# Kernel tuning notes

Measured on AMD Instinct MI355X. Metric: run time of the kernel, lower is better.

## Reference

```python
import jax, jax.numpy as jnp
import numpy as np

L, E, H, S, V, F = 8, 1024, 16, 2048, 32000, 4096
NEG = -1e9  # mask value used by the original (triu * -1e9)


def setup_inputs() -> dict:
    key = jax.random.key(0)
    ks = jax.random.split(key, 10)
    s = 0.02  # init scale to keep activations stable without residuals/LN
    return {
        "inpt": jax.random.randint(ks[0], (S,), 0, V, dtype=jnp.int32),
        "num_heads": H,
        "emb_table": jax.random.normal(ks[1], (V, E), dtype=jnp.float32) * s,
        "Wq": jax.random.normal(ks[2], (L, E, E), dtype=jnp.float32) * s,
        "bq": jnp.zeros((L, E), dtype=jnp.float32),
        "Wk": jax.random.normal(ks[3], (L, E, E), dtype=jnp.float32) * s,
        "bk": jnp.zeros((L, E), dtype=jnp.float32),
        "Wv": jax.random.normal(ks[4], (L, E, E), dtype=jnp.float32) * s,
        "bv": jnp.zeros((L, E), dtype=jnp.float32),
        "W1": jax.random.normal(ks[5], (L, E, F), dtype=jnp.float32) * s,
        "b1": jnp.zeros((L, F), dtype=jnp.float32),
        "W2": jax.random.normal(ks[6], (L, F, E), dtype=jnp.float32) * s,
        "b2": jnp.zeros((L, E), dtype=jnp.float32),
        "Wout": jax.random.normal(ks[7], (E, V), dtype=jnp.float32) * s,
    }


def reference(inpt, num_heads, emb_table, Wq, bq, Wk, bk, Wv, bv, W1, b1, W2, b2, Wout):
    x = emb_table[inpt]                      # [S, E] embedding lookup
    seq_len, emb_dim = x.shape
    head_dim = emb_dim // num_heads
    scale = head_dim ** 0.5
    n_layers = Wq.shape[0]
    # additive causal mask, exactly as torch.triu(ones)*-1e9
    mask = jnp.triu(jnp.full((seq_len, seq_len), NEG, dtype=x.dtype), k=1)

    for l in range(n_layers):  # fixed small layer count
        q = (x @ Wq[l] + bq[l]).reshape(seq_len, num_heads, head_dim).transpose(1, 0, 2)
        k = (x @ Wk[l] + bk[l]).reshape(seq_len, num_heads, head_dim).transpose(1, 0, 2)
        v = (x @ Wv[l] + bv[l]).reshape(seq_len, num_heads, head_dim).transpose(1, 0, 2)
        scores = jnp.einsum('hqd,hkd->hqk', q, k) / scale + mask  # [H, S, S]
        probs = jax.nn.softmax(scores, axis=-1)
        attn = jnp.einsum('hqk,hkd->hqd', probs, v)               # [H, S, D]
        attn = attn.transpose(1, 0, 2).reshape(seq_len, emb_dim)  # [S, E]
        # NOTE: original has no residual connection; x is replaced by FFN(attn)
        x = jax.nn.relu(attn @ W1[l] + b1[l]) @ W2[l] + b2[l]

    return x @ Wout  # [S, V] logits (no bias, no softmax in original forward)
```

## Files before the change

kernel.cpp:

```cpp
#include <hip/hip_runtime.h>
#include <hip/hip_fp16.h>


#define SS 2048
#define EE 1024
#define NH 16
#define FF 4096
#define NV 32000
#define NL 8

typedef _Float16 f16;
typedef _Float16 f16x8 __attribute__((ext_vector_type(8)));
typedef _Float16 f16x4 __attribute__((ext_vector_type(4)));
typedef float f32x4 __attribute__((ext_vector_type(4)));
typedef float f32x16 __attribute__((ext_vector_type(16)));

#define CS 4096.0f
#define INV_CS 0.000244140625f
#define SCORE_SCALE 7.450580596923828e-09f

__device__ __forceinline__ void gload16(const void* g, void* lds) {
    __builtin_amdgcn_global_load_lds(
        (const __attribute__((address_space(1))) unsigned int*)g,
        (__attribute__((address_space(3))) unsigned int*)lds, 16, 0, 0);
}

#define BAR do { asm volatile("" ::: "memory"); __builtin_amdgcn_s_barrier(); } while (0)

__global__ void k_embed(const int* __restrict__ ids, const float* __restrict__ emb,
                        f16* __restrict__ xh) {
    int s = blockIdx.x;
    int e = threadIdx.x * 4;
    const float4 v = *(const float4*)&emb[(size_t)ids[s] * EE + e];
    f16x4 h;
    h[0] = (f16)(v.x * CS); h[1] = (f16)(v.y * CS);
    h[2] = (f16)(v.z * CS); h[3] = (f16)(v.w * CS);
    *(f16x4*)&xh[(size_t)s * EE + e] = h;
}

__device__ __forceinline__ void tr64(const float* __restrict__ in, f16* __restrict__ out,
                                     int ldi, int ldo, int bx, int by) {
    __shared__ float tl[64][65];
    const int tx = threadIdx.x & 15, ty = threadIdx.x >> 4;
#pragma unroll
    for (int i = 0; i < 4; i++) {
        float4 v = *(const float4*)&in[(size_t)(by + ty * 4 + i) * ldi + bx + tx * 4];
        tl[ty * 4 + i][tx * 4 + 0] = v.x;
        tl[ty * 4 + i][tx * 4 + 1] = v.y;
        tl[ty * 4 + i][tx * 4 + 2] = v.z;
        tl[ty * 4 + i][tx * 4 + 3] = v.w;
    }
    __syncthreads();
#pragma unroll
    for (int i = 0; i < 4; i++) {
        f16x4 h;
#pragma unroll
        for (int j = 0; j < 4; j++) h[j] = (f16)tl[tx * 4 + j][ty * 4 + i];
        *(f16x4*)&out[(size_t)(bx + ty * 4 + i) * ldo + by + tx * 4] = h;
    }
}

__global__ void k_trW(const float* __restrict__ Wq, const float* __restrict__ Wk,
                      const float* __restrict__ Wv, const float* __restrict__ W1,
                      const float* __restrict__ W2,
                      const float* __restrict__ bq, const float* __restrict__ bk,
                      const float* __restrict__ bv,
                      f16* __restrict__ wqkvt, f16* __restrict__ w1t,
                      f16* __restrict__ w2t, float* __restrict__ bqkv) {
    int b = blockIdx.x;
    if (b == 2816) {
        int i = threadIdx.x;
#pragma unroll
        for (int j = 0; j < 12; j++) {
            int idx = j * 256 + i;
            bqkv[idx] = idx < EE ? bq[idx] : (idx < 2 * EE ? bk[idx - EE] : bv[idx - 2 * EE]);
        }
        return;
    }
    if (b < 768) {
        int s = b >> 8, t2 = b & 255;
        tr64(s == 0 ? Wq : (s == 1 ? Wk : Wv), wqkvt + (size_t)s * EE * EE,
             EE, EE, (t2 & 15) * 64, (t2 >> 4) * 64);
    } else if (b < 1792) {
        int t2 = b - 768;
        tr64(W1, w1t, FF, EE, (t2 & 63) * 64, (t2 >> 6) * 64);
    } else {
        int t2 = b - 1792;
        tr64(W2, w2t, EE, FF, (t2 & 15) * 64, (t2 >> 4) * 64);
    }
}

__global__ void k_trOut(const float* __restrict__ in, f16* __restrict__ out) {
    int b = blockIdx.x;
    tr64(in, out, NV, EE, (b % 500) * 64, (b / 500) * 64);
}

__global__ void k_combine4(const float* __restrict__ part, const float* __restrict__ bias,
                           f16* __restrict__ out) {
    const size_t sz = (size_t)SS * EE;
    int i = (blockIdx.x * 256 + threadIdx.x) * 4;
    float4 a = *(const float4*)&part[i];
    float4 b = *(const float4*)&part[i + sz];
    float4 c = *(const float4*)&part[i + 2 * sz];
    float4 d = *(const float4*)&part[i + 3 * sz];
    float4 bb = *(const float4*)&bias[i & (EE - 1)];
    f16x4 h;
    h[0] = (f16)(a.x + b.x + c.x + d.x + bb.x * CS);
    h[1] = (f16)(a.y + b.y + c.y + d.y + bb.y * CS);
    h[2] = (f16)(a.z + b.z + c.z + d.z + bb.z * CS);
    h[3] = (f16)(a.w + b.w + c.w + d.w + bb.w * CS);
    *(f16x4*)&out[i] = h;
}

template<int BM, int BN, int TAG>
__global__ __launch_bounds__((BM == 128) ? 256 : 512, 2) void k_gemm(
    const f16* __restrict__ A, const f16* __restrict__ B,
    const float* __restrict__ bias, f16* __restrict__ Ch, float* __restrict__ Cf,
    f16* __restrict__ VtOut,
    int M, int N, int Kstride, int Ksub, int nm, int nn, int kch,
    float bscale, float oscale, int relu) {
    constexpr int WR = (BM == 256) ? ((BN == 256) ? 2 : 4) : 2;
    constexpr int WC = (BN == 256) ? 4 : 2;
    constexpr int NW = WR * WC;
    constexpr int THREADS = NW * 64;
    constexpr int MR = BM / WR / 16;
    constexpr int RPC = THREADS / 8;
    constexpr int ACALLS = BM / RPC;
    constexpr int BCALLS = BN / RPC;
    constexpr int LPT = ACALLS + BCALLS;

    __shared__ f16 As[2][BM * 64];
    __shared__ f16 Bs[2][BN * 64];

    const int t = threadIdx.x;
    const int l = t & 63, w = t >> 6;
    const int lr = l & 15, lc = l >> 4;

    const int nwg = nm * nn * kch;
    const int q8 = nwg >> 3, r8 = nwg & 7;
    const int xcd = blockIdx.x & 7, lid = blockIdx.x >> 3;
    const int wgid = (xcd < r8 ? xcd * (q8 + 1) : r8 * (q8 + 1) + (xcd - r8) * q8) + lid;
    const int kc = wgid / (nm * nn);
    const int rem = wgid - kc * (nm * nn);
    const int m0 = (rem % nm) * BM, n0 = (rem / nm) * BN;

    const f16* Ab = A + (size_t)kc * Ksub;
    const f16* Bb = B + (size_t)kc * Ksub;
    float* Cfb = Cf ? Cf + (size_t)kc * M * N : nullptr;

    const int wr = w / WC, wc = w % WC;

    f32x4 acc[MR][4] = {};

    const int srow = t >> 3;
    const int scol = 8 * ((t & 7) ^ (srow & 7));
    const int NT = Ksub / 64;

#define STAGE(bb, tt_) { \
    const size_t kof = (size_t)(tt_) * 64 + scol; \
    _Pragma("unroll") \
    for (int c = 0; c < ACALLS; c++) \
        gload16(Ab + (size_t)(m0 + c * RPC + srow) * Kstride + kof, \
                (char*)As[bb] + c * (RPC * 128) + w * 1024); \
    _Pragma("unroll") \
    for (int c = 0; c < BCALLS; c++) \
        gload16(Bb + (size_t)(n0 + c * RPC + srow) * Kstride + kof, \
                (char*)Bs[bb] + c * (RPC * 128) + w * 1024); }

    STAGE(0, 0)
    STAGE(1, 1)
    asm volatile("s_waitcnt vmcnt(%0)" :: "n"(LPT) : "memory");
    BAR;

    int cur = 0;
    for (int tt = 0; tt < NT; ++tt) {
        const f16* pA = As[cur];
        const f16* pB = Bs[cur];
#pragma unroll
        for (int ks = 0; ks < 2; ks++) {
            f16x8 af[MR], bf[4];
#pragma unroll
            for (int m = 0; m < MR; m++) {
                const int row = wr * (MR * 16) + m * 16 + lr;
                af[m] = *(const f16x8*)&pA[row * 64 + 8 * ((ks * 4 + lc) ^ (row & 7))];
            }
#pragma unroll
            for (int n = 0; n < 4; n++) {
                const int row = wc * 64 + n * 16 + lr;
                bf[n] = *(const f16x8*)&pB[row * 64 + 8 * ((ks * 4 + lc) ^ (row & 7))];
            }
            __builtin_amdgcn_s_setprio(1);
#pragma unroll
            for (int m = 0; m < MR; m++)
#pragma unroll
                for (int n = 0; n < 4; n++)
                    acc[m][n] = __builtin_amdgcn_mfma_f32_16x16x32_f16(af[m], bf[n], acc[m][n], 0, 0, 0);
            __builtin_amdgcn_s_setprio(0);
        }
        BAR;
        if (tt + 2 < NT) {
            STAGE(cur, tt + 2)
            asm volatile("s_waitcnt vmcnt(%0)" :: "n"(LPT) : "memory");
        } else if (tt + 1 < NT) {
            asm volatile("s_waitcnt vmcnt(0)" ::: "memory");
        }
        BAR;
        cur ^= 1;
    }
#undef STAGE

#pragma unroll
    for (int m = 0; m < MR; m++)
#pragma unroll
        for (int n = 0; n < 4; n++) {
            const int row0 = m0 + wr * (MR * 16) + m * 16 + lc * 4;
            const int col = n0 + wc * 64 + n * 16 + lr;
            float v[4];
#pragma unroll
            for (int r = 0; r < 4; r++) {
                v[r] = acc[m][n][r];
                if (bias) v[r] += bias[col] * bscale;
                if (relu) v[r] = fmaxf(v[r], 0.0f);
            }
            if (VtOut && col >= 2 * EE) {
                f16x4 h4;
#pragma unroll
                for (int r = 0; r < 4; r++) h4[r] = (f16)v[r];
                *(f16x4*)&VtOut[(size_t)(col - 2 * EE) * SS + row0] = h4;
            } else if (Ch) {
#pragma unroll
                for (int r = 0; r < 4; r++)
                    Ch[(size_t)(row0 + r) * N + col] = (f16)v[r];
            } else {
#pragma unroll
                for (int r = 0; r < 4; r++)
                    Cfb[(size_t)(row0 + r) * N + col] = v[r] * oscale;
            }
        }
}

__global__ __launch_bounds__(512, 2) void k_gemm32(
    const f16* __restrict__ A, const f16* __restrict__ B, float* __restrict__ Cf,
    int N, int Kstride, int nm, int nn, float oscale) {
    __shared__ f16 As[2][256 * 64];
    __shared__ f16 Bs[2][256 * 64];
    const int t = threadIdx.x;
    const int l = t & 63, w = t >> 6;
    const int ln = l & 31, hi = l >> 5;

    const int nwg = nm * nn;
    const int q8 = nwg >> 3, r8 = nwg & 7;
    const int xcd = blockIdx.x & 7, lid = blockIdx.x >> 3;
    const int wgid = (xcd < r8 ? xcd * (q8 + 1) : r8 * (q8 + 1) + (xcd - r8) * q8) + lid;
    const int m0 = (wgid % nm) * 256, n0 = (wgid / nm) * 256;

    const int wr = w >> 2, wc = w & 3;
    f32x16 acc[4][2] = {};

    const int srow = t >> 3;
    const int scol = 8 * ((t & 7) ^ (srow & 7));
    const int NT = Kstride / 64;

#define STAGE32(bb, tt_) { \
    const size_t kof = (size_t)(tt_) * 64 + scol; \
    _Pragma("unroll") \
    for (int c = 0; c < 4; c++) { \
        gload16(A + (size_t)(m0 + c * 64 + srow) * Kstride + kof, \
                (char*)As[bb] + c * 8192 + w * 1024); \
        gload16(B + (size_t)(n0 + c * 64 + srow) * Kstride + kof, \
                (char*)Bs[bb] + c * 8192 + w * 1024); } }

    STAGE32(0, 0)
    STAGE32(1, 1)
    asm volatile("s_waitcnt vmcnt(8)" ::: "memory");
    BAR;

    int cur = 0;
    for (int tt = 0; tt < NT; ++tt) {
        const f16* pA = As[cur];
        const f16* pB = Bs[cur];
#pragma unroll
        for (int ks = 0; ks < 4; ks++) {
            f16x8 af[4], bf[2];
#pragma unroll
            for (int m = 0; m < 4; m++) {
                const int row = wr * 128 + m * 32 + ln;
                af[m] = *(const f16x8*)&pA[row * 64 + 8 * ((ks * 2 + hi) ^ (row & 7))];
            }
#pragma unroll
            for (int n = 0; n < 2; n++) {
                const int row = wc * 64 + n * 32 + ln;
                bf[n] = *(const f16x8*)&pB[row * 64 + 8 * ((ks * 2 + hi) ^ (row & 7))];
            }
            __builtin_amdgcn_s_setprio(1);
#pragma unroll
            for (int m = 0; m < 4; m++)
#pragma unroll
                for (int n = 0; n < 2; n++)
                    acc[m][n] = __builtin_amdgcn_mfma_f32_32x32x16_f16(af[m], bf[n], acc[m][n], 0, 0, 0);
            __builtin_amdgcn_s_setprio(0);
        }
        BAR;
        if (tt + 2 < NT) {
            STAGE32(cur, tt + 2)
            asm volatile("s_waitcnt vmcnt(8)" ::: "memory");
        } else if (tt + 1 < NT) {
            asm volatile("s_waitcnt vmcnt(0)" ::: "memory");
        }
        BAR;
        cur ^= 1;
    }
#undef STAGE32

#pragma unroll
    for (int m = 0; m < 4; m++)
#pragma unroll
        for (int n = 0; n < 2; n++)
#pragma unroll
            for (int r = 0; r < 16; r++) {
                const int row = m0 + wr * 128 + m * 32 + (r & 3) + 8 * (r >> 2) + 4 * hi;
                const int col = n0 + wc * 64 + n * 32 + ln;
                Cf[(size_t)row * N + col] = acc[m][n][r] * oscale;
            }
}

__global__ __launch_bounds__(256) void k_flash(
    const f16* __restrict__ qkv, const f16* __restrict__ vt, f16* __restrict__ attn) {
    __shared__ f16 Ks[2][4096];
    __shared__ f16 Vs[2][4096];
    __shared__ f16 Ps[4096];
    const int h = blockIdx.x;
    const int qb = (SS / 64 - 1) - blockIdx.y;
    const int t = threadIdx.x, l = t & 63, w = t >> 6;
    const int lr = l & 15, lc = l >> 4;
    const int q0 = qb * 64;
    const int qrow = q0 + w * 16 + lr;

    f16x8 qf0 = *(const f16x8*)&qkv[(size_t)qrow * 3072 + h * 64 + lc * 8];
    f16x8 qf1 = *(const f16x8*)&qkv[(size_t)qrow * 3072 + h * 64 + 32 + lc * 8];

    f32x4 o[4] = {};
    float mrun[4], lrun[4];
#pragma unroll
    for (int r = 0; r < 4; r++) { mrun[r] = -__builtin_inff(); lrun[r] = 0.0f; }

    const int krow = t >> 3;
    const int kscol = 8 * ((t & 7) ^ (krow & 7));
    const f16* gK = qkv + EE + h * 64;
    const f16* gV = vt + (size_t)(h * 64) * SS;
    f16* Pw = &Ps[w * 16 * 64];
    const int psw = (lr & 7) << 4;

#define FSTAGE(bb, kt_) { \
    char* dK = (char*)Ks[bb] + w * 1024; \
    char* dV = (char*)Vs[bb] + w * 1024; \
    gload16(gK + (size_t)((kt_) * 64 + krow) * 3072 + kscol, dK); \
    gload16(gK + (size_t)((kt_) * 64 + krow + 32) * 3072 + kscol, dK + 4096); \
    gload16(gV + (size_t)krow * SS + (kt_) * 64 + kscol, dV); \
    gload16(gV + (size_t)(krow + 32) * SS + (kt_) * 64 + kscol, dV + 4096); }

    const int nkt = qb + 1;
    FSTAGE(0, 0)
    FSTAGE(1, 1)
    asm volatile("s_waitcnt vmcnt(4)" ::: "memory");
    __builtin_amdgcn_s_barrier();

    int cur = 0;
    for (int kt = 0; kt < nkt; kt++) {
        f32x4 sc[4];
        __builtin_amdgcn_s_setprio(1);
#pragma unroll
        for (int kj = 0; kj < 4; kj++) {
            const int krw = kj * 16 + lr;
            const int sw = krw & 7;
            f16x8 kb0 = *(const f16x8*)&Ks[cur][krw * 64 + 8 * (lc ^ sw)];
            f16x8 kb1 = *(const f16x8*)&Ks[cur][krw * 64 + 8 * ((lc + 4) ^ sw)];
            f32x4 z = {};
            z = __builtin_amdgcn_mfma_f32_16x16x32_f16(qf0, kb0, z, 0, 0, 0);
            z = __builtin_amdgcn_mfma_f32_16x16x32_f16(qf1, kb1, z, 0, 0, 0);
            sc[kj] = z;
        }
        __builtin_amdgcn_s_setprio(0);

        const bool diag = (kt == qb);
#pragma unroll
        for (int kj = 0; kj < 4; kj++)
#pragma unroll
            for (int r = 0; r < 4; r++) {
                float v = sc[kj][r] * SCORE_SCALE;
                if (diag) {
                    int qq = w * 16 + lc * 4 + r;
                    int kk = kj * 16 + lr;
                    if (kk > qq) v = -__builtin_inff();
                }
                sc[kj][r] = v;
            }

#pragma unroll
        for (int r = 0; r < 4; r++) {
            float mt = fmaxf(fmaxf(sc[0][r], sc[1][r]), fmaxf(sc[2][r], sc[3][r]));
            mt = fmaxf(mt, __shfl_xor(mt, 1));
            mt = fmaxf(mt, __shfl_xor(mt, 2));
            mt = fmaxf(mt, __shfl_xor(mt, 4));
            mt = fmaxf(mt, __shfl_xor(mt, 8));
            float mnew = fmaxf(mrun[r], mt);
            float alpha = __expf(mrun[r] - mnew);
            float psum = 0.0f;
#pragma unroll
            for (int kj = 0; kj < 4; kj++) {
                float p = __expf(sc[kj][r] - mnew);
                sc[kj][r] = p;
                psum += p;
            }
            psum += __shfl_xor(psum, 1);
            psum += __shfl_xor(psum, 2);
            psum += __shfl_xor(psum, 4);
            psum += __shfl_xor(psum, 8);
            lrun[r] = lrun[r] * alpha + psum;
            mrun[r] = mnew;
#pragma unroll
            for (int dj = 0; dj < 4; dj++) o[dj][r] *= alpha;
        }

#pragma unroll
        for (int kj = 0; kj < 4; kj++)
#pragma unroll
            for (int r = 0; r < 4; r++) {
                int prow = lc * 4 + r;
                int pb = prow * 128 + ((kj * 16 + lr) * 2 ^ ((prow & 7) << 4));
                *(f16*)((char*)Pw + pb) = (f16)sc[kj][r];
            }

        __builtin_amdgcn_s_setprio(1);
#pragma unroll
        for (int s2 = 0; s2 < 2; s2++) {
            f16x8 pa = *(const f16x8*)((const char*)Pw + lr * 128 + (((lc + 4 * s2) * 16) ^ psw));
#pragma unroll
            for (int dj = 0; dj < 4; dj++) {
                const int vrow = dj * 16 + lr;
                f16x8 vb = *(const f16x8*)&Vs[cur][vrow * 64 + 8 * ((lc + 4 * s2) ^ (vrow & 7))];
                o[dj] = __builtin_amdgcn_mfma_f32_16x16x32_f16(pa, vb, o[dj], 0, 0, 0);
            }
        }
        __builtin_amdgcn_s_setprio(0);

        asm volatile("" ::: "memory");
        __builtin_amdgcn_s_barrier();
        if (kt + 2 < nkt) {
            FSTAGE(cur, kt + 2)
            asm volatile("s_waitcnt vmcnt(4)" ::: "memory");
        } else if (kt + 1 < nkt) {
            asm volatile("s_waitcnt vmcnt(0)" ::: "memory");
        }
        __builtin_amdgcn_s_barrier();
        cur ^= 1;
    }
#undef FSTAGE

#pragma unroll
    for (int dj = 0; dj < 4; dj++)
#pragma unroll
        for (int r = 0; r < 4; r++) {
            float v = o[dj][r] / lrun[r];
            attn[(size_t)(q0 + w * 16 + lc * 4 + r) * EE + h * 64 + dj * 16 + lr] = (f16)v;
        }
}

extern "C" void kernel_launch(void* const* d_in, const int* in_sizes, int n_in,
                              void* d_out, int out_size, void* d_ws, size_t ws_size,
                              hipStream_t stream) {
    const int*   ids  = (const int*)d_in[0];
    const float* emb  = (const float*)d_in[2];
    const float* Wq   = (const float*)d_in[3];
    const float* bq   = (const float*)d_in[4];
    const float* Wk   = (const float*)d_in[5];
    const float* bk   = (const float*)d_in[6];
    const float* Wv   = (const float*)d_in[7];
    const float* bv   = (const float*)d_in[8];
    const float* W1   = (const float*)d_in[9];
    const float* b1   = (const float*)d_in[10];
    const float* W2   = (const float*)d_in[11];
    const float* b2   = (const float*)d_in[12];
    const float* Wout = (const float*)d_in[13];
    float* out = (float*)d_out;

    char* p = (char*)d_ws;
    f16* xh    = (f16*)p; p += (size_t)SS * EE * 2;
    f16* qkvh  = (f16*)p; p += (size_t)SS * 3 * EE * 2;
    f16* vt    = (f16*)p; p += (size_t)EE * SS * 2;
    f16* attn  = (f16*)p; p += (size_t)SS * EE * 2;
    f16* h1    = (f16*)p; p += (size_t)SS * FF * 2;
    f16* wqkvt = (f16*)p; p += (size_t)3 * EE * EE * 2;
    f16* w1t   = (f16*)p; p += (size_t)FF * EE * 2;
    f16* w2t   = (f16*)p; p += (size_t)EE * FF * 2;
    f16* woutt = (f16*)p; p += (size_t)NV * EE * 2;
    float* part = (float*)p; p += (size_t)4 * SS * EE * 4;
    float* bqkv = (float*)p; p += 3 * EE * 4;

    k_embed<<<SS, 256, 0, stream>>>(ids, emb, xh);

    for (int l = 0; l < NL; l++) {
        k_trW<<<2817, 256, 0, stream>>>(
            Wq + (size_t)l * EE * EE, Wk + (size_t)l * EE * EE, Wv + (size_t)l * EE * EE,
            W1 + (size_t)l * EE * FF, W2 + (size_t)l * FF * EE,
            bq + l * EE, bk + l * EE, bv + l * EE,
            wqkvt, w1t, w2t, bqkv);

        k_gemm<256, 128, 1><<<8 * 24, 512, 0, stream>>>(
            xh, wqkvt, bqkv, qkvh, nullptr, vt, SS, 3 * EE, EE, EE, 8, 24, 1, CS, 1.0f, 0);

        k_flash<<<dim3(NH, SS / 64), 256, 0, stream>>>(qkvh, vt, attn);

        k_gemm<256, 128, 2><<<8 * 32, 512, 0, stream>>>(
            attn, w1t, b1 + (size_t)l * FF, h1, nullptr, nullptr, SS, FF, EE, EE, 8, 32, 1, CS, 1.0f, 1);

        k_gemm<256, 128, 3><<<8 * 8 * 4, 512, 0, stream>>>(
            h1, w2t, nullptr, nullptr, part, nullptr, SS, EE, FF, FF / 4, 8, 8, 4, 0.0f, 1.0f, 0);
        k_combine4<<<SS * EE / 1024, 256, 0, stream>>>(part, b2 + (size_t)l * EE, xh);
    }

    k_trOut<<<8000, 256, 0, stream>>>(Wout, woutt);
    k_gemm32<<<8 * 125, 512, 0, stream>>>(xh, woutt, out, NV, EE, 8, 125, INV_CS);
}
```

Baseline: 1.540 ms.

## Rewrite output GEMM as four-phase pipelined 16x16 MFMA kernel

The final vocabulary-projection GEMM switches from 32x32x16 MFMAs to 16x16x32 MFMAs. The per-tile loop is split into four barrier-separated phases that interleave LDS fragment loads, pieces of the next tile's global-to-LDS staging, and MFMA blocks. The aim is to overlap memory traffic with matrix math and reduce stalls in this large GEMM. The cost is more barriers per K-tile and a different accumulator layout, which may raise register pressure.

```diff
diff --git a/kernel.cpp b/kernel.cpp
--- a/kernel.cpp
+++ b/kernel.cpp
@@ -13,7 +13,6 @@
 typedef _Float16 f16x8 __attribute__((ext_vector_type(8)));
 typedef _Float16 f16x4 __attribute__((ext_vector_type(4)));
 typedef float f32x4 __attribute__((ext_vector_type(4)));
-typedef float f32x16 __attribute__((ext_vector_type(16)));
 
 #define CS 4096.0f
 #define INV_CS 0.000244140625f
@@ -239,14 +238,14 @@
         }
 }
 
-__global__ __launch_bounds__(512, 2) void k_gemm32(
+__global__ __launch_bounds__(512, 2) void k_gemm4p(
     const f16* __restrict__ A, const f16* __restrict__ B, float* __restrict__ Cf,
-    int N, int Kstride, int nm, int nn, float oscale) {
+    int N, int K, int nm, int nn, float oscale) {
     __shared__ f16 As[2][256 * 64];
     __shared__ f16 Bs[2][256 * 64];
     const int t = threadIdx.x;
     const int l = t & 63, w = t >> 6;
-    const int ln = l & 31, hi = l >> 5;
+    const int lr = l & 15, lc = l >> 4;
 
     const int nwg = nm * nn;
     const int q8 = nwg >> 3, r8 = nwg & 7;
@@ -255,23 +254,45 @@
     const int m0 = (wgid % nm) * 256, n0 = (wgid / nm) * 256;
 
     const int wr = w >> 2, wc = w & 3;
-    f32x16 acc[4][2] = {};
+
+    f32x4 acc[8][4] = {};
+    f16x8 aF[2][4], bF[2][4];
 
     const int srow = t >> 3;
     const int scol = 8 * ((t & 7) ^ (srow & 7));
-    const int NT = Kstride / 64;
-
-#define STAGE32(bb, tt_) { \
-    const size_t kof = (size_t)(tt_) * 64 + scol; \
-    _Pragma("unroll") \
-    for (int c = 0; c < 4; c++) { \
-        gload16(A + (size_t)(m0 + c * 64 + srow) * Kstride + kof, \
-                (char*)As[bb] + c * 8192 + w * 1024); \
-        gload16(B + (size_t)(n0 + c * 64 + srow) * Kstride + kof, \
-                (char*)Bs[bb] + c * 8192 + w * 1024); } }
-
-    STAGE32(0, 0)
-    STAGE32(1, 1)
+    const int NT = K / 64;
+
+#define SG_A(bb, tt_, c) \
+    gload16(A + (size_t)(m0 + (c) * 64 + srow) * K + (size_t)(tt_) * 64 + scol, \
+            (char*)As[bb] + (c) * 8192 + w * 1024);
+#define SG_B(bb, tt_, c) \
+    gload16(B + (size_t)(n0 + (c) * 64 + srow) * K + (size_t)(tt_) * 64 + scol, \
+            (char*)Bs[bb] + (c) * 8192 + w * 1024);
+
+#define LDA_HALF(pA_, mh) { _Pragma("unroll") \
+    for (int ks = 0; ks < 2; ks++) _Pragma("unroll") \
+    for (int m = 0; m < 4; m++) { \
+        const int row = wr * 128 + ((mh) * 4 + m) * 16 + lr; \
+        aF[ks][m] = *(const f16x8*)&pA_[row * 64 + 8 * ((ks * 4 + lc) ^ (row & 7))]; } }
+
+#define LDB_PAIR(pB_, nb) { _Pragma("unroll") \
+    for (int ks = 0; ks < 2; ks++) _Pragma("unroll") \
+    for (int j = 0; j < 2; j++) { \
+        const int row = wc * 64 + ((nb) + j) * 16 + lr; \
+        bF[ks][(nb) + j] = *(const f16x8*)&pB_[row * 64 + 8 * ((ks * 4 + lc) ^ (row & 7))]; } }
+
+#define PH_MMA(mb, nb) { __builtin_amdgcn_s_setprio(1); \
+    _Pragma("unroll") for (int ks = 0; ks < 2; ks++) \
+    _Pragma("unroll") for (int m = 0; m < 4; m++) \
+    _Pragma("unroll") for (int j = 0; j < 2; j++) \
+        acc[(mb) + m][(nb) + j] = __builtin_amdgcn_mfma_f32_16x16x32_f16( \
+            aF[ks][m], bF[ks][(nb) + j], acc[(mb) + m][(nb) + j], 0, 0, 0); \
+    __builtin_amdgcn_s_setprio(0); }
+
+#pragma unroll
+    for (int c = 0; c < 4; c++) { SG_A(0, 0, c) SG_B(0, 0, c) }
+#pragma unroll
+    for (int c = 0; c < 4; c++) { SG_A(1, 1, c) SG_B(1, 1, c) }
     asm volatile("s_waitcnt vmcnt(8)" ::: "memory");
     BAR;
 
@@ -279,49 +300,55 @@
     for (int tt = 0; tt < NT; ++tt) {
         const f16* pA = As[cur];
         const f16* pB = Bs[cur];
-#pragma unroll
-        for (int ks = 0; ks < 4; ks++) {
-            f16x8 af[4], bf[2];
-#pragma unroll
-            for (int m = 0; m < 4; m++) {
-                const int row = wr * 128 + m * 32 + ln;
-                af[m] = *(const f16x8*)&pA[row * 64 + 8 * ((ks * 2 + hi) ^ (row & 7))];
-            }
-#pragma unroll
-            for (int n = 0; n < 2; n++) {
-                const int row = wc * 64 + n * 32 + ln;
-                bf[n] = *(const f16x8*)&pB[row * 64 + 8 * ((ks * 2 + hi) ^ (row & 7))];
-            }
-            __builtin_amdgcn_s_setprio(1);
-#pragma unroll
-            for (int m = 0; m < 4; m++)
-#pragma unroll
-                for (int n = 0; n < 2; n++)
-                    acc[m][n] = __builtin_amdgcn_mfma_f32_32x32x16_f16(af[m], bf[n], acc[m][n], 0, 0, 0);
-            __builtin_amdgcn_s_setprio(0);
-        }
-        BAR;
-        if (tt + 2 < NT) {
-            STAGE32(cur, tt + 2)
+        const bool pre = (tt + 2 < NT);
+
+        LDA_HALF(pA, 0)
+        LDB_PAIR(pB, 0)
+        BAR;
+        PH_MMA(0, 0)
+        BAR;
+
+        LDB_PAIR(pB, 2)
+        if (pre) { SG_A(cur, tt + 2, 0) SG_A(cur, tt + 2, 2) }
+        BAR;
+        PH_MMA(0, 2)
+        BAR;
+
+        LDA_HALF(pA, 1)
+        if (pre) { SG_B(cur, tt + 2, 0) SG_B(cur, tt + 2, 1)
+                   SG_B(cur, tt + 2, 2) SG_B(cur, tt + 2, 3) }
+        BAR;
+        PH_MMA(4, 0)
+        BAR;
+
+        if (pre) {
+            SG_A(cur, tt + 2, 1) SG_A(cur, tt + 2, 3)
             asm volatile("s_waitcnt vmcnt(8)" ::: "memory");
         } else if (tt + 1 < NT) {
             asm volatile("s_waitcnt vmcnt(0)" ::: "memory");
         }
         BAR;
+        PH_MMA(4, 2)
+        BAR;
+
         cur ^= 1;
     }
-#undef STAGE32
-
-#pragma unroll
-    for (int m = 0; m < 4; m++)
-#pragma unroll
-        for (int n = 0; n < 2; n++)
-#pragma unroll
-            for (int r = 0; r < 16; r++) {
-                const int row = m0 + wr * 128 + m * 32 + (r & 3) + 8 * (r >> 2) + 4 * hi;
-                const int col = n0 + wc * 64 + n * 32 + ln;
-                Cf[(size_t)row * N + col] = acc[m][n][r] * oscale;
-            }
+#undef SG_A
+#undef SG_B
+#undef LDA_HALF
+#undef LDB_PAIR
+#undef PH_MMA
+
+#pragma unroll
+    for (int m = 0; m < 8; m++)
+#pragma unroll
+        for (int n = 0; n < 4; n++) {
+            const int row0 = m0 + wr * 128 + m * 16 + lc * 4;
+            const int col = n0 + wc * 64 + n * 16 + lr;
+#pragma unroll
+            for (int r = 0; r < 4; r++)
+                Cf[(size_t)(row0 + r) * N + col] = acc[m][n][r] * oscale;
+        }
 }
 
 __global__ __launch_bounds__(256) void k_flash(
@@ -520,5 +547,5 @@
     }
 
     k_trOut<<<8000, 256, 0, stream>>>(Wout, woutt);
-    k_gemm32<<<8 * 125, 512, 0, stream>>>(xh, woutt, out, NV, EE, 8, 125, INV_CS);
-}
+    k_gemm4p<<<8 * 125, 512, 0, stream>>>(xh, woutt, out, NV, EE, 8, 125, INV_CS);
+}
```

After: 1.523 ms. No clear change (-1.1%).
